# Kernel optimization log

Measured on AMD Instinct MI355X. Metric: run time of the kernel, lower is better.

## Reference

```python
import jax, jax.numpy as jnp
import numpy as np

EMB_DIM = 1024
N_HEADS = 16
HEAD_DIM = EMB_DIM // N_HEADS


def setup_inputs() -> dict:
    key = jax.random.key(0)
    ks = jax.random.split(key, 6)
    B, T, C = 2, 2048, EMB_DIM
    s = 1.0 / np.sqrt(C)
    return {
        "x": jax.random.normal(ks[0], (B, T, C), dtype=jnp.float32),
        "W_query": jax.random.normal(ks[1], (C, C), dtype=jnp.float32) * s,
        "W_key": jax.random.normal(ks[2], (C, C), dtype=jnp.float32) * s,
        "W_value": jax.random.normal(ks[3], (C, C), dtype=jnp.float32) * s,
        "W_out": jax.random.normal(ks[4], (C, C), dtype=jnp.float32) * s,
        "b_out": jax.random.normal(ks[5], (C,), dtype=jnp.float32) * 0.01,
    }


def reference(x, W_query, W_key, W_value, W_out, b_out):
    # x: [B, T, C]. Linear weights stored as [in, out] (transposed torch layout).
    B, T, C = x.shape
    H, D = N_HEADS, HEAD_DIM

    def split_heads(t):  # [B,T,C] -> [B,H,T,D]
        return t.reshape(B, T, H, D).transpose(0, 2, 1, 3)

    q = split_heads(x @ W_query)
    k = split_heads(x @ W_key)
    v = split_heads(x @ W_value)

    scale = 1.0 / jnp.sqrt(jnp.asarray(D, dtype=x.dtype))
    att = jnp.einsum("bhqd,bhkd->bhqk", q, k) * scale  # [B,H,T,T]
    causal = jnp.tril(jnp.ones((T, T), dtype=bool))
    att = jnp.where(causal[None, None], att, jnp.asarray(-jnp.inf, dtype=att.dtype))
    att = jax.nn.softmax(att, axis=-1)
    # dropout is identity in eval / drop_rate=0
    y = jnp.einsum("bhqk,bhkd->bhqd", att, v)  # [B,H,T,D]
    y = y.transpose(0, 2, 1, 3).reshape(B, T, C)
    return y @ W_out + b_out
```

## Files before the change

### kernel.cpp

```cpp
#include <hip/hip_runtime.h>
#include <hip/hip_bf16.h>
#include <math.h>

#define Bsz 2
#define Tsz 2048
#define Csz 1024
#define Hsz 16
#define Dsz 64

typedef __attribute__((ext_vector_type(8))) short frag8;
typedef __attribute__((ext_vector_type(4))) float f4;
typedef __attribute__((ext_vector_type(8))) unsigned short us8;
typedef __attribute__((ext_vector_type(4))) _Float16 frag4h;
typedef __attribute__((ext_vector_type(8))) _Float16 frag8h;

static __device__ __forceinline__ unsigned short f2bf(float f) {
  union { __hip_bfloat16 h; unsigned short u; } c;
  c.h = __float2bfloat16(f);
  return c.u;
}
static __device__ __forceinline__ unsigned short f2h(float f) {
  union { _Float16 h; unsigned short u; } c;
  c.h = (_Float16)f;
  return c.u;
}

#define GLDS16(g, l)                                                        \
  __builtin_amdgcn_global_load_lds(                                         \
      (const __attribute__((address_space(1))) void*)(g),                   \
      (__attribute__((address_space(3))) void*)(l), 16, 0, 0)

#define QSCALE 0.18033688f

__global__ __launch_bounds__(256) void cast_x(const float* __restrict__ x,
                                              unsigned short* __restrict__ xb) {
  const int i = (blockIdx.x * 256 + threadIdx.x) * 8;
  const float4 a = *(const float4*)(x + i);
  const float4 b = *(const float4*)(x + i + 4);
  us8 v;
  v[0] = f2bf(a.x); v[1] = f2bf(a.y); v[2] = f2bf(a.z); v[3] = f2bf(a.w);
  v[4] = f2bf(b.x); v[5] = f2bf(b.y); v[6] = f2bf(b.z); v[7] = f2bf(b.w);
  *(us8*)(xb + i) = v;
}

__global__ __launch_bounds__(256) void transpose_cast(
    const float* __restrict__ s0, const float* __restrict__ s1,
    const float* __restrict__ s2, const float* __restrict__ s3,
    unsigned short* __restrict__ d0, unsigned short* __restrict__ d1,
    unsigned short* __restrict__ d2, unsigned short* __restrict__ d3) {
  __shared__ float Ls[64][65];
  const int mat = blockIdx.x >> 8;
  const int tile = blockIdx.x & 255;
  const float* src = mat == 0 ? s0 : mat == 1 ? s1 : mat == 2 ? s2 : s3;
  unsigned short* dst = mat == 0 ? d0 : mat == 1 ? d1 : mat == 2 ? d2 : d3;
  const int tr0 = (tile >> 4) << 6, tc0 = (tile & 15) << 6;
  const int t = threadIdx.x;
  const int lr = t >> 4, lc = (t & 15) << 2;
#pragma unroll
  for (int j = 0; j < 4; ++j) {
    const float4 v = *(const float4*)(src + (size_t)(tr0 + lr + j * 16) * 1024 + tc0 + lc);
    Ls[lr + j * 16][lc + 0] = v.x;
    Ls[lr + j * 16][lc + 1] = v.y;
    Ls[lr + j * 16][lc + 2] = v.z;
    Ls[lr + j * 16][lc + 3] = v.w;
  }
  __syncthreads();
#pragma unroll
  for (int j = 0; j < 4; ++j) {
    ushort4 v;
    v.x = f2bf(Ls[lc + 0][lr + j * 16]);
    v.y = f2bf(Ls[lc + 1][lr + j * 16]);
    v.z = f2bf(Ls[lc + 2][lr + j * 16]);
    v.w = f2bf(Ls[lc + 3][lr + j * 16]);
    *(ushort4*)(dst + (size_t)(tc0 + lr + j * 16) * 1024 + tr0 + lc) = v;
  }
}

template <int MODE, int MT>
__global__ __launch_bounds__(256) void mm_bt(
    const unsigned short* __restrict__ A, const unsigned short* __restrict__ Bt,
    const float* __restrict__ bias, unsigned short* __restrict__ O0,
    unsigned short* __restrict__ O1, unsigned short* __restrict__ O2,
    float* __restrict__ Of) {
  __shared__ __align__(16) unsigned short As[MT * 32 * 64];
  __shared__ __align__(16) unsigned short Bs[128 * 64];
  const int K = 1024;
  const int tid = threadIdx.x;
  const int wave = tid >> 6, lane = tid & 63;
  const int quad = lane >> 4, l16 = lane & 15;
  const int wrow = (wave >> 1) * (MT * 16), wn = wave & 1;
  const int row0 = blockIdx.y * (MT * 32), col0 = blockIdx.x << 7;

  const int sr = lane >> 3, sg = lane & 7;
  const int g0 = sg ^ sr;
  const unsigned short* gA = A + (size_t)(row0 + wave * (MT * 8) + sr) * K + (g0 << 3);
  const unsigned short* gB = Bt + (size_t)(col0 + wave * 32 + sr) * K + (g0 << 3);

  f4 acc[MT][4];
#pragma unroll
  for (int i = 0; i < MT; ++i)
#pragma unroll
    for (int j = 0; j < 4; ++j) acc[i][j] = (f4){0.f, 0.f, 0.f, 0.f};

  for (int kk = 0; kk < K; kk += 64) {
    __syncthreads();
#pragma unroll
    for (int s = 0; s < MT; ++s)
      GLDS16(gA + kk + (size_t)(s * 8) * K, &As[(wave * (MT * 8) + s * 8) * 64]);
#pragma unroll
    for (int s = 0; s < 4; ++s)
      GLDS16(gB + kk + (size_t)(s * 8) * K, &Bs[(wave * 32 + s * 8) * 64]);
    __syncthreads();

#pragma unroll
    for (int ks = 0; ks < 2; ++ks) {
      frag8 af[MT], bf[4];
#pragma unroll
      for (int mt = 0; mt < MT; ++mt) {
        const int r = wrow + mt * 16 + l16;
        af[mt] = *(const frag8*)&As[r * 64 + (((ks * 4 + quad) ^ (l16 & 7)) << 3)];
      }
#pragma unroll
      for (int nt = 0; nt < 4; ++nt) {
        const int n = wn * 64 + nt * 16 + l16;
        bf[nt] = *(const frag8*)&Bs[n * 64 + (((ks * 4 + quad) ^ (l16 & 7)) << 3)];
      }
#pragma unroll
      for (int mt = 0; mt < MT; ++mt)
#pragma unroll
        for (int nt = 0; nt < 4; ++nt)
          acc[mt][nt] = __builtin_amdgcn_mfma_f32_16x16x32_bf16(af[mt], bf[nt], acc[mt][nt], 0, 0, 0);
    }
  }

  if (MODE == 0) {
    if (col0 < 2048) {
      const bool isK = (col0 >= 1024);
      unsigned short* dst = isK ? O1 : O0;
      const float sc = isK ? 1.0f : QSCALE;
#pragma unroll
      for (int mt = 0; mt < MT; ++mt)
#pragma unroll
        for (int nt = 0; nt < 4; ++nt) {
          const int m = row0 + wrow + mt * 16 + quad * 4;
          const int n = (col0 & 1023) + wn * 64 + nt * 16 + l16;
          const int b = m >> 11, h = n >> 6, d = n & 63;
#pragma unroll
          for (int r = 0; r < 4; ++r) {
            const int tk = (m + r) & (Tsz - 1);
            dst[(((size_t)b * Hsz + h) * Tsz + tk) * Dsz + d] = f2bf(acc[mt][nt][r] * sc);
          }
        }
    } else {
#pragma unroll
      for (int mt = 0; mt < MT; ++mt)
#pragma unroll
        for (int nt = 0; nt < 4; ++nt) {
          const int tok = row0 + wrow + mt * 16 + quad * 4;
          const int ch = (col0 - 2048) + wn * 64 + nt * 16 + l16;
          const int b = tok >> 11, tk = tok & (Tsz - 1);
          const int h = ch >> 6, d = ch & 63;
          const int t5 = tk & 31;
          const int pos = (tk & ~31) + ((t5 >> 4) << 2) + (((t5 >> 2) & 3) << 3) + (t5 & 3);
          ushort4 v;
          v.x = f2h(acc[mt][nt][0]); v.y = f2h(acc[mt][nt][1]);
          v.z = f2h(acc[mt][nt][2]); v.w = f2h(acc[mt][nt][3]);
          *(ushort4*)&O2[(((size_t)b * Hsz + h) * Dsz + d) * Tsz + pos] = v;
        }
    }
  } else {
#pragma unroll
    for (int mt = 0; mt < MT; ++mt)
#pragma unroll
      for (int nt = 0; nt < 4; ++nt) {
        const int m = row0 + wrow + mt * 16 + quad * 4;
        const int n = col0 + wn * 64 + nt * 16 + l16;
        const float bv = bias[n];
#pragma unroll
        for (int r = 0; r < 4; ++r)
          Of[(size_t)(m + r) * Csz + n] = acc[mt][nt][r] + bv;
      }
  }
}

__global__ __launch_bounds__(512, 4) void attn_mfma(
    const unsigned short* __restrict__ Qb,
    const unsigned short* __restrict__ Kb,
    const unsigned short* __restrict__ VTb,
    unsigned short* __restrict__ Y) {
  __shared__ __align__(16) unsigned char SMEM[65536];
#define KSP(spp, bb) ((unsigned short*)(SMEM + (spp) * 16384 + (bb) * 4096))
#define VSP(spp, bb) ((unsigned short*)(SMEM + (spp) * 16384 + 8192 + (bb) * 4096))

  const int tid = threadIdx.x;
  const int wave = tid >> 6, lane = tid & 63;
  const int quad = lane >> 4, l16 = lane & 15;
  const int t = wave & 1;
  const int sp = wave >> 1;
  const int ltid = tid & 127;

  const int bh = blockIdx.x & 31;
  const int pr = blockIdx.x >> 5;
  const int ja = pr, jb = 63 - pr;
  const int j = t ? jb : ja;
  const int qb0 = j << 5;

  const unsigned short* Qh = Qb + (size_t)bh * Tsz * Dsz;
  const unsigned short* Kh = Kb + (size_t)bh * Tsz * Dsz;
  const unsigned short* Vh = VTb + (size_t)bh * Dsz * Tsz;

  const int ke0 = ltid, ke1 = ltid + 128;
  const int kkey0 = ke0 >> 3, kc0 = ke0 & 7;
  const int kkey1 = ke1 >> 3, kc1 = ke1 & 7;
  const unsigned short* gK0 = Kh + (size_t)kkey0 * Dsz + ((kc0 ^ (kkey0 & 7)) << 3);
  const unsigned short* gK1 = Kh + (size_t)kkey1 * Dsz + ((kc1 ^ (kkey1 & 7)) << 3);
  const int vd0 = ltid >> 2, vc0 = ltid & 3;
  const int vd1 = vd0 + 32;
  const unsigned short* gV0 = Vh + (size_t)vd0 * Tsz + ((vc0 ^ ((vd0 + (vd0 >> 2)) & 3)) << 3);
  const unsigned short* gV1 = Vh + (size_t)vd1 * Tsz + ((vc0 ^ ((vd1 + (vd1 >> 2)) & 3)) << 3);
  const int wo = t * 512;

  frag8 qf[2][2];
#pragma unroll
  for (int m = 0; m < 2; ++m)
#pragma unroll
    for (int ks = 0; ks < 2; ++ks)
      qf[m][ks] = *(const frag8*)(Qh + (size_t)(qb0 + m * 16 + l16) * Dsz + ks * 32 + quad * 8);

  f4 o[2][4];
  float lsum[2] = {0.f, 0.f};
#pragma unroll
  for (int m = 0; m < 2; ++m)
#pragma unroll
    for (int nt = 0; nt < 4; ++nt) o[m][nt] = (f4){0.f, 0.f, 0.f, 0.f};
  const f4 zf = (f4){0.f, 0.f, 0.f, 0.f};
  const int fl = (l16 + (l16 >> 2)) & 3;

  const int nch = (jb >> 2) + 1;

  {
    const size_t kof0 = (size_t)(sp << 5) * Dsz, kof1 = (size_t)((sp + 4) << 5) * Dsz;
    const int vof0 = sp << 5, vof1 = (sp + 4) << 5;
    GLDS16(gK0 + kof0, KSP(sp, 0) + wo);
    GLDS16(gK1 + kof0, KSP(sp, 0) + wo + 1024);
    GLDS16(gV0 + vof0, VSP(sp, 0) + wo);
    GLDS16(gV1 + vof0, VSP(sp, 0) + wo + 1024);
    GLDS16(gK0 + kof1, KSP(sp, 1) + wo);
    GLDS16(gK1 + kof1, KSP(sp, 1) + wo + 1024);
    GLDS16(gV0 + vof1, VSP(sp, 1) + wo);
    GLDS16(gV1 + vof1, VSP(sp, 1) + wo + 1024);
  }
  __syncthreads();

  for (int i = 0; i < nch; ++i) {
    const int c = sp + 4 * i;
    const int bsel = i & 1;
    if (c <= j) {
      const unsigned short* Kl = KSP(sp, bsel);
      const unsigned short* Vl = VSP(sp, bsel);
      frag8 kf[2][2];
#pragma unroll
      for (int n = 0; n < 2; ++n)
#pragma unroll
        for (int ks = 0; ks < 2; ++ks)
          kf[n][ks] = *(const frag8*)&Kl[(n * 16 + l16) * 64 + (((ks * 4 + quad) ^ (l16 & 7)) << 3)];
      frag8h vf[4];
#pragma unroll
      for (int nt = 0; nt < 4; ++nt)
        vf[nt] = *(const frag8h*)&Vl[(nt * 16 + l16) * 32 + ((quad ^ fl) << 3)];

      f4 st[2][2];
#pragma unroll
      for (int n = 0; n < 2; ++n)
#pragma unroll
        for (int m = 0; m < 2; ++m) {
          f4 a = __builtin_amdgcn_mfma_f32_16x16x32_bf16(kf[n][0], qf[m][0], zf, 0, 0, 0);
          st[n][m] = __builtin_amdgcn_mfma_f32_16x16x32_bf16(kf[n][1], qf[m][1], a, 0, 0, 0);
        }
      const bool dm = (c == j);
      frag4h paf[2][2];
#pragma unroll
      for (int m = 0; m < 2; ++m) {
        const int qq = m * 16 + l16;
#pragma unroll
        for (int n = 0; n < 2; ++n) {
          const int key0 = n * 16 + quad * 4;
          float p[4];
#pragma unroll
          for (int r = 0; r < 4; ++r) {
            float sv = st[n][m][r];
            if (dm && (key0 + r > qq)) sv = -INFINITY;
            p[r] = __builtin_amdgcn_exp2f(sv);
          }
          lsum[m] += (p[0] + p[1]) + (p[2] + p[3]);
          frag4h ph;
          ph[0] = (_Float16)p[0]; ph[1] = (_Float16)p[1];
          ph[2] = (_Float16)p[2]; ph[3] = (_Float16)p[3];
          paf[m][n] = ph;
        }
      }
#pragma unroll
      for (int m = 0; m < 2; ++m)
#pragma unroll
        for (int nt = 0; nt < 4; ++nt) {
          const frag4h vlo = __builtin_shufflevector(vf[nt], vf[nt], 0, 1, 2, 3);
          const frag4h vhi = __builtin_shufflevector(vf[nt], vf[nt], 4, 5, 6, 7);
          f4 a = __builtin_amdgcn_mfma_f32_16x16x16f16(paf[m][0], vlo, o[m][nt], 0, 0, 0);
          o[m][nt] = __builtin_amdgcn_mfma_f32_16x16x16f16(paf[m][1], vhi, a, 0, 0, 0);
        }
    }
    __syncthreads();
    if (i + 2 < nch) {
      const int c2 = sp + 4 * (i + 2);
      const size_t kof = (size_t)(c2 << 5) * Dsz;
      const int vof = c2 << 5;
      GLDS16(gK0 + kof, KSP(sp, bsel) + wo);
      GLDS16(gK1 + kof, KSP(sp, bsel) + wo + 1024);
      GLDS16(gV0 + vof, VSP(sp, bsel) + wo);
      GLDS16(gV1 + vof, VSP(sp, bsel) + wo + 1024);
    }
  }

  float* comb = (float*)SMEM;
  const int slot = (sp - 1) * 2 + t;
  float* cp = comb + (size_t)(slot * 64 + lane) * 37;
  if (sp != 0) {
#pragma unroll
    for (int m = 0; m < 2; ++m)
#pragma unroll
      for (int nt = 0; nt < 4; ++nt)
        *(f4*)(cp + m * 16 + nt * 4) = o[m][nt];
    cp[32] = lsum[0]; cp[33] = lsum[1];
  }
  __syncthreads();
  if (sp == 0) {
#pragma unroll
    for (int s = 0; s < 3; ++s) {
      const float* rp = comb + (size_t)((s * 2 + t) * 64 + lane) * 37;
#pragma unroll
      for (int m = 0; m < 2; ++m)
#pragma unroll
        for (int nt = 0; nt < 4; ++nt)
          o[m][nt] += *(const f4*)(rp + m * 16 + nt * 4);
      lsum[0] += rp[32]; lsum[1] += rp[33];
    }

#pragma unroll
    for (int m = 0; m < 2; ++m) {
      lsum[m] += __shfl_xor(lsum[m], 16);
      lsum[m] += __shfl_xor(lsum[m], 32);
    }
    const int b = bh >> 4, h = bh & 15;
#pragma unroll
    for (int m = 0; m < 2; ++m)
#pragma unroll
      for (int r = 0; r < 4; ++r) {
        const float inv = 1.f / __shfl(lsum[m], quad * 4 + r);
        const int tk = qb0 + m * 16 + quad * 4 + r;
        unsigned short* yp = Y + ((size_t)b * Tsz + tk) * Csz + h * 64 + l16;
#pragma unroll
        for (int nt = 0; nt < 4; ++nt)
          yp[nt * 16] = f2bf(o[m][nt][r] * inv);
      }
  }
#undef KSP
#undef VSP
}

extern "C" void kernel_launch(void* const* d_in, const int* in_sizes, int n_in,
                              void* d_out, int out_size, void* d_ws, size_t ws_size,
                              hipStream_t stream) {
  const float* x  = (const float*)d_in[0];
  const float* Wq = (const float*)d_in[1];
  const float* Wk = (const float*)d_in[2];
  const float* Wv = (const float*)d_in[3];
  const float* Wo = (const float*)d_in[4];
  const float* bo = (const float*)d_in[5];

  const size_t NEL = (size_t)Bsz * Tsz * Csz;
  const size_t WSZ = (size_t)Csz * Csz;
  unsigned short* xb  = (unsigned short*)d_ws;
  unsigned short* WT  = xb + NEL;
  unsigned short* WoT = WT + 3 * WSZ;
  unsigned short* Qb  = WoT + WSZ;
  unsigned short* Kb  = Qb + NEL;
  unsigned short* VTb = Kb + NEL;
  unsigned short* Yb  = VTb + NEL;

  cast_x<<<NEL / 2048, 256, 0, stream>>>(x, xb);
  transpose_cast<<<1024, 256, 0, stream>>>(Wq, Wk, Wv, Wo,
                                           WT, WT + WSZ, WT + 2 * WSZ, WoT);

  mm_bt<0, 4><<<dim3(24, 32), 256, 0, stream>>>(xb, WT, nullptr, Qb, Kb, VTb, nullptr);

  attn_mfma<<<1024, 512, 0, stream>>>(Qb, Kb, VTb, Yb);

  mm_bt<2, 2><<<dim3(8, 64), 256, 0, stream>>>(Yb, WoT, bo, nullptr, nullptr, nullptr,
                                               (float*)d_out);
}
```

Before: 182.5 us.

## Load K/V fragments directly from global memory, dropping LDS double buffering

The attention kernel stops staging K and V chunks through LDS with async global_load_lds double buffering and per-iteration block barriers. Each wave now loads its MFMA K and V fragments straight from global memory (relying on cache), and the loop runs only over the chunks that wave needs. LDS shrinks to just the cross-wave combine buffer. The wave-to-(t,sp) mapping changes, and P is packed to f16 with cvt_pkrtz. This removes barrier stalls and LDS traffic but exposes global-load latency with no explicit prefetch, and it uses less coalesced fragment-shaped accesses.

Result: slower. 225.7 us (+23.7%).

```diff
diff --git a/kernel.cpp b/kernel.cpp
--- a/kernel.cpp
+++ b/kernel.cpp
@@ -13,6 +13,7 @@
 typedef __attribute__((ext_vector_type(8))) unsigned short us8;
 typedef __attribute__((ext_vector_type(4))) _Float16 frag4h;
 typedef __attribute__((ext_vector_type(8))) _Float16 frag8h;
+typedef __attribute__((ext_vector_type(2))) _Float16 h2;
 
 static __device__ __forceinline__ unsigned short f2bf(float f) {
   union { __hip_bfloat16 h; unsigned short u; } c;
@@ -188,16 +189,13 @@
     const unsigned short* __restrict__ Kb,
     const unsigned short* __restrict__ VTb,
     unsigned short* __restrict__ Y) {
-  __shared__ __align__(16) unsigned char SMEM[65536];
-#define KSP(spp, bb) ((unsigned short*)(SMEM + (spp) * 16384 + (bb) * 4096))
-#define VSP(spp, bb) ((unsigned short*)(SMEM + (spp) * 16384 + 8192 + (bb) * 4096))
+  __shared__ __align__(16) float comb[6 * 64 * 37];
 
   const int tid = threadIdx.x;
   const int wave = tid >> 6, lane = tid & 63;
   const int quad = lane >> 4, l16 = lane & 15;
-  const int t = wave & 1;
-  const int sp = wave >> 1;
-  const int ltid = tid & 127;
+  const int t = wave >> 2;
+  const int sp = wave & 3;
 
   const int bh = blockIdx.x & 31;
   const int pr = blockIdx.x >> 5;
@@ -209,17 +207,6 @@
   const unsigned short* Kh = Kb + (size_t)bh * Tsz * Dsz;
   const unsigned short* Vh = VTb + (size_t)bh * Dsz * Tsz;
 
-  const int ke0 = ltid, ke1 = ltid + 128;
-  const int kkey0 = ke0 >> 3, kc0 = ke0 & 7;
-  const int kkey1 = ke1 >> 3, kc1 = ke1 & 7;
-  const unsigned short* gK0 = Kh + (size_t)kkey0 * Dsz + ((kc0 ^ (kkey0 & 7)) << 3);
-  const unsigned short* gK1 = Kh + (size_t)kkey1 * Dsz + ((kc1 ^ (kkey1 & 7)) << 3);
-  const int vd0 = ltid >> 2, vc0 = ltid & 3;
-  const int vd1 = vd0 + 32;
-  const unsigned short* gV0 = Vh + (size_t)vd0 * Tsz + ((vc0 ^ ((vd0 + (vd0 >> 2)) & 3)) << 3);
-  const unsigned short* gV1 = Vh + (size_t)vd1 * Tsz + ((vc0 ^ ((vd1 + (vd1 >> 2)) & 3)) << 3);
-  const int wo = t * 512;
-
   frag8 qf[2][2];
 #pragma unroll
   for (int m = 0; m < 2; ++m)
@@ -234,94 +221,62 @@
 #pragma unroll
     for (int nt = 0; nt < 4; ++nt) o[m][nt] = (f4){0.f, 0.f, 0.f, 0.f};
   const f4 zf = (f4){0.f, 0.f, 0.f, 0.f};
-  const int fl = (l16 + (l16 >> 2)) & 3;
-
-  const int nch = (jb >> 2) + 1;
-
-  {
-    const size_t kof0 = (size_t)(sp << 5) * Dsz, kof1 = (size_t)((sp + 4) << 5) * Dsz;
-    const int vof0 = sp << 5, vof1 = (sp + 4) << 5;
-    GLDS16(gK0 + kof0, KSP(sp, 0) + wo);
-    GLDS16(gK1 + kof0, KSP(sp, 0) + wo + 1024);
-    GLDS16(gV0 + vof0, VSP(sp, 0) + wo);
-    GLDS16(gV1 + vof0, VSP(sp, 0) + wo + 1024);
-    GLDS16(gK0 + kof1, KSP(sp, 1) + wo);
-    GLDS16(gK1 + kof1, KSP(sp, 1) + wo + 1024);
-    GLDS16(gV0 + vof1, VSP(sp, 1) + wo);
-    GLDS16(gV1 + vof1, VSP(sp, 1) + wo + 1024);
-  }
-  __syncthreads();
-
-  for (int i = 0; i < nch; ++i) {
-    const int c = sp + 4 * i;
-    const int bsel = i & 1;
-    if (c <= j) {
-      const unsigned short* Kl = KSP(sp, bsel);
-      const unsigned short* Vl = VSP(sp, bsel);
-      frag8 kf[2][2];
-#pragma unroll
-      for (int n = 0; n < 2; ++n)
-#pragma unroll
-        for (int ks = 0; ks < 2; ++ks)
-          kf[n][ks] = *(const frag8*)&Kl[(n * 16 + l16) * 64 + (((ks * 4 + quad) ^ (l16 & 7)) << 3)];
-      frag8h vf[4];
-#pragma unroll
-      for (int nt = 0; nt < 4; ++nt)
-        vf[nt] = *(const frag8h*)&Vl[(nt * 16 + l16) * 32 + ((quad ^ fl) << 3)];
-
-      f4 st[2][2];
-#pragma unroll
-      for (int n = 0; n < 2; ++n)
-#pragma unroll
-        for (int m = 0; m < 2; ++m) {
-          f4 a = __builtin_amdgcn_mfma_f32_16x16x32_bf16(kf[n][0], qf[m][0], zf, 0, 0, 0);
-          st[n][m] = __builtin_amdgcn_mfma_f32_16x16x32_bf16(kf[n][1], qf[m][1], a, 0, 0, 0);
+
+  const unsigned short* kl = Kh + (size_t)l16 * Dsz + quad * 8;
+  const unsigned short* vl = Vh + (size_t)l16 * Tsz + quad * 8;
+
+  for (int c = sp; c <= j; c += 4) {
+    frag8 kf[2][2];
+#pragma unroll
+    for (int n = 0; n < 2; ++n)
+#pragma unroll
+      for (int ks = 0; ks < 2; ++ks)
+        kf[n][ks] = *(const frag8*)(kl + (size_t)(c * 32 + n * 16) * Dsz + ks * 32);
+    frag8h vf[4];
+#pragma unroll
+    for (int nt = 0; nt < 4; ++nt)
+      vf[nt] = *(const frag8h*)(vl + (size_t)(nt * 16) * Tsz + (c << 5));
+
+    f4 st[2][2];
+#pragma unroll
+    for (int n = 0; n < 2; ++n)
+#pragma unroll
+      for (int m = 0; m < 2; ++m) {
+        f4 a = __builtin_amdgcn_mfma_f32_16x16x32_bf16(kf[n][0], qf[m][0], zf, 0, 0, 0);
+        st[n][m] = __builtin_amdgcn_mfma_f32_16x16x32_bf16(kf[n][1], qf[m][1], a, 0, 0, 0);
+      }
+    const bool dm = (c == j);
+    frag4h paf[2][2];
+#pragma unroll
+    for (int m = 0; m < 2; ++m) {
+      const int qq = m * 16 + l16;
+#pragma unroll
+      for (int n = 0; n < 2; ++n) {
+        const int key0 = n * 16 + quad * 4;
+        float p[4];
+#pragma unroll
+        for (int r = 0; r < 4; ++r) {
+          float sv = st[n][m][r];
+          if (dm && (key0 + r > qq)) sv = -INFINITY;
+          p[r] = __builtin_amdgcn_exp2f(sv);
         }
-      const bool dm = (c == j);
-      frag4h paf[2][2];
-#pragma unroll
-      for (int m = 0; m < 2; ++m) {
-        const int qq = m * 16 + l16;
-#pragma unroll
-        for (int n = 0; n < 2; ++n) {
-          const int key0 = n * 16 + quad * 4;
-          float p[4];
-#pragma unroll
-          for (int r = 0; r < 4; ++r) {
-            float sv = st[n][m][r];
-            if (dm && (key0 + r > qq)) sv = -INFINITY;
-            p[r] = __builtin_amdgcn_exp2f(sv);
-          }
-          lsum[m] += (p[0] + p[1]) + (p[2] + p[3]);
-          frag4h ph;
-          ph[0] = (_Float16)p[0]; ph[1] = (_Float16)p[1];
-          ph[2] = (_Float16)p[2]; ph[3] = (_Float16)p[3];
-          paf[m][n] = ph;
-        }
-      }
-#pragma unroll
-      for (int m = 0; m < 2; ++m)
-#pragma unroll
-        for (int nt = 0; nt < 4; ++nt) {
-          const frag4h vlo = __builtin_shufflevector(vf[nt], vf[nt], 0, 1, 2, 3);
-          const frag4h vhi = __builtin_shufflevector(vf[nt], vf[nt], 4, 5, 6, 7);
-          f4 a = __builtin_amdgcn_mfma_f32_16x16x16f16(paf[m][0], vlo, o[m][nt], 0, 0, 0);
-          o[m][nt] = __builtin_amdgcn_mfma_f32_16x16x16f16(paf[m][1], vhi, a, 0, 0, 0);
-        }
-    }
-    __syncthreads();
-    if (i + 2 < nch) {
-      const int c2 = sp + 4 * (i + 2);
-      const size_t kof = (size_t)(c2 << 5) * Dsz;
-      const int vof = c2 << 5;
-      GLDS16(gK0 + kof, KSP(sp, bsel) + wo);
-      GLDS16(gK1 + kof, KSP(sp, bsel) + wo + 1024);
-      GLDS16(gV0 + vof, VSP(sp, bsel) + wo);
-      GLDS16(gV1 + vof, VSP(sp, bsel) + wo + 1024);
-    }
-  }
-
-  float* comb = (float*)SMEM;
+        lsum[m] += (p[0] + p[1]) + (p[2] + p[3]);
+        const h2 lo = __builtin_bit_cast(h2, __builtin_amdgcn_cvt_pkrtz(p[0], p[1]));
+        const h2 hi = __builtin_bit_cast(h2, __builtin_amdgcn_cvt_pkrtz(p[2], p[3]));
+        paf[m][n] = __builtin_shufflevector(lo, hi, 0, 1, 2, 3);
+      }
+    }
+#pragma unroll
+    for (int m = 0; m < 2; ++m)
+#pragma unroll
+      for (int nt = 0; nt < 4; ++nt) {
+        const frag4h vlo = __builtin_shufflevector(vf[nt], vf[nt], 0, 1, 2, 3);
+        const frag4h vhi = __builtin_shufflevector(vf[nt], vf[nt], 4, 5, 6, 7);
+        f4 a = __builtin_amdgcn_mfma_f32_16x16x16f16(paf[m][0], vlo, o[m][nt], 0, 0, 0);
+        o[m][nt] = __builtin_amdgcn_mfma_f32_16x16x16f16(paf[m][1], vhi, a, 0, 0, 0);
+      }
+  }
+
   const int slot = (sp - 1) * 2 + t;
   float* cp = comb + (size_t)(slot * 64 + lane) * 37;
   if (sp != 0) {
@@ -363,8 +318,6 @@
           yp[nt * 16] = f2bf(o[m][nt][r] * inv);
       }
   }
-#undef KSP
-#undef VSP
 }
 
 extern "C" void kernel_launch(void* const* d_in, const int* in_sizes, int n_in,
```

## Split both causal query tiles across wave pair to balance work

Applied to the files above, without the earlier changes.

Previously each wave pair had one wave handle the short query tile (ja) and the other the long tile (jb), so one wave sat idle for most chunks. Now each wave takes 16 query rows from both tiles: it always computes the jb tile and also the ja tile while the chunk is within its range. This evens out work between waves and shortens the critical path per block. In exchange each wave holds more registers for two accumulator sets, and the reduction and store code are reorganised to match.

New measurement: 180.7 us. Within noise of the previous version (-1.0%).

```diff
diff --git a/kernel.cpp b/kernel.cpp
--- a/kernel.cpp
+++ b/kernel.cpp
@@ -202,8 +202,7 @@
   const int bh = blockIdx.x & 31;
   const int pr = blockIdx.x >> 5;
   const int ja = pr, jb = 63 - pr;
-  const int j = t ? jb : ja;
-  const int qb0 = j << 5;
+  const int qa0 = ja << 5, qb0 = jb << 5;
 
   const unsigned short* Qh = Qb + (size_t)bh * Tsz * Dsz;
   const unsigned short* Kh = Kb + (size_t)bh * Tsz * Dsz;
@@ -220,21 +219,23 @@
   const unsigned short* gV1 = Vh + (size_t)vd1 * Tsz + ((vc0 ^ ((vd1 + (vd1 >> 2)) & 3)) << 3);
   const int wo = t * 512;
 
-  frag8 qf[2][2];
-#pragma unroll
-  for (int m = 0; m < 2; ++m)
-#pragma unroll
-    for (int ks = 0; ks < 2; ++ks)
-      qf[m][ks] = *(const frag8*)(Qh + (size_t)(qb0 + m * 16 + l16) * Dsz + ks * 32 + quad * 8);
-
-  f4 o[2][4];
-  float lsum[2] = {0.f, 0.f};
-#pragma unroll
-  for (int m = 0; m < 2; ++m)
-#pragma unroll
-    for (int nt = 0; nt < 4; ++nt) o[m][nt] = (f4){0.f, 0.f, 0.f, 0.f};
+  frag8 qfa[2], qfb[2];
+#pragma unroll
+  for (int ks = 0; ks < 2; ++ks) {
+    qfa[ks] = *(const frag8*)(Qh + (size_t)(qa0 + t * 16 + l16) * Dsz + ks * 32 + quad * 8);
+    qfb[ks] = *(const frag8*)(Qh + (size_t)(qb0 + t * 16 + l16) * Dsz + ks * 32 + quad * 8);
+  }
+
+  f4 oa[4], ob[4];
+  float lsa = 0.f, lsb = 0.f;
+#pragma unroll
+  for (int nt = 0; nt < 4; ++nt) {
+    oa[nt] = (f4){0.f, 0.f, 0.f, 0.f};
+    ob[nt] = (f4){0.f, 0.f, 0.f, 0.f};
+  }
   const f4 zf = (f4){0.f, 0.f, 0.f, 0.f};
   const int fl = (l16 + (l16 >> 2)) & 3;
+  const int qq = t * 16 + l16;
 
   const int nch = (jb >> 2) + 1;
 
@@ -255,7 +256,7 @@
   for (int i = 0; i < nch; ++i) {
     const int c = sp + 4 * i;
     const int bsel = i & 1;
-    if (c <= j) {
+    if (c <= jb) {
       const unsigned short* Kl = KSP(sp, bsel);
       const unsigned short* Vl = VSP(sp, bsel);
       frag8 kf[2][2];
@@ -269,45 +270,72 @@
       for (int nt = 0; nt < 4; ++nt)
         vf[nt] = *(const frag8h*)&Vl[(nt * 16 + l16) * 32 + ((quad ^ fl) << 3)];
 
-      f4 st[2][2];
-#pragma unroll
-      for (int n = 0; n < 2; ++n)
-#pragma unroll
-        for (int m = 0; m < 2; ++m) {
-          f4 a = __builtin_amdgcn_mfma_f32_16x16x32_bf16(kf[n][0], qf[m][0], zf, 0, 0, 0);
-          st[n][m] = __builtin_amdgcn_mfma_f32_16x16x32_bf16(kf[n][1], qf[m][1], a, 0, 0, 0);
-        }
-      const bool dm = (c == j);
-      frag4h paf[2][2];
-#pragma unroll
-      for (int m = 0; m < 2; ++m) {
-        const int qq = m * 16 + l16;
+      {
+        f4 st[2];
+#pragma unroll
+        for (int n = 0; n < 2; ++n) {
+          f4 a = __builtin_amdgcn_mfma_f32_16x16x32_bf16(kf[n][0], qfb[0], zf, 0, 0, 0);
+          st[n] = __builtin_amdgcn_mfma_f32_16x16x32_bf16(kf[n][1], qfb[1], a, 0, 0, 0);
+        }
+        const bool dm = (c == jb);
+        frag4h paf[2];
 #pragma unroll
         for (int n = 0; n < 2; ++n) {
           const int key0 = n * 16 + quad * 4;
           float p[4];
 #pragma unroll
           for (int r = 0; r < 4; ++r) {
-            float sv = st[n][m][r];
+            float sv = st[n][r];
             if (dm && (key0 + r > qq)) sv = -INFINITY;
             p[r] = __builtin_amdgcn_exp2f(sv);
           }
-          lsum[m] += (p[0] + p[1]) + (p[2] + p[3]);
+          lsb += (p[0] + p[1]) + (p[2] + p[3]);
           frag4h ph;
           ph[0] = (_Float16)p[0]; ph[1] = (_Float16)p[1];
           ph[2] = (_Float16)p[2]; ph[3] = (_Float16)p[3];
-          paf[m][n] = ph;
-        }
-      }
-#pragma unroll
-      for (int m = 0; m < 2; ++m)
+          paf[n] = ph;
+        }
 #pragma unroll
         for (int nt = 0; nt < 4; ++nt) {
           const frag4h vlo = __builtin_shufflevector(vf[nt], vf[nt], 0, 1, 2, 3);
           const frag4h vhi = __builtin_shufflevector(vf[nt], vf[nt], 4, 5, 6, 7);
-          f4 a = __builtin_amdgcn_mfma_f32_16x16x16f16(paf[m][0], vlo, o[m][nt], 0, 0, 0);
-          o[m][nt] = __builtin_amdgcn_mfma_f32_16x16x16f16(paf[m][1], vhi, a, 0, 0, 0);
-        }
+          f4 a = __builtin_amdgcn_mfma_f32_16x16x16f16(paf[0], vlo, ob[nt], 0, 0, 0);
+          ob[nt] = __builtin_amdgcn_mfma_f32_16x16x16f16(paf[1], vhi, a, 0, 0, 0);
+        }
+      }
+      if (c <= ja) {
+        f4 st[2];
+#pragma unroll
+        for (int n = 0; n < 2; ++n) {
+          f4 a = __builtin_amdgcn_mfma_f32_16x16x32_bf16(kf[n][0], qfa[0], zf, 0, 0, 0);
+          st[n] = __builtin_amdgcn_mfma_f32_16x16x32_bf16(kf[n][1], qfa[1], a, 0, 0, 0);
+        }
+        const bool dm = (c == ja);
+        frag4h paf[2];
+#pragma unroll
+        for (int n = 0; n < 2; ++n) {
+          const int key0 = n * 16 + quad * 4;
+          float p[4];
+#pragma unroll
+          for (int r = 0; r < 4; ++r) {
+            float sv = st[n][r];
+            if (dm && (key0 + r > qq)) sv = -INFINITY;
+            p[r] = __builtin_amdgcn_exp2f(sv);
+          }
+          lsa += (p[0] + p[1]) + (p[2] + p[3]);
+          frag4h ph;
+          ph[0] = (_Float16)p[0]; ph[1] = (_Float16)p[1];
+          ph[2] = (_Float16)p[2]; ph[3] = (_Float16)p[3];
+          paf[n] = ph;
+        }
+#pragma unroll
+        for (int nt = 0; nt < 4; ++nt) {
+          const frag4h vlo = __builtin_shufflevector(vf[nt], vf[nt], 0, 1, 2, 3);
+          const frag4h vhi = __builtin_shufflevector(vf[nt], vf[nt], 4, 5, 6, 7);
+          f4 a = __builtin_amdgcn_mfma_f32_16x16x16f16(paf[0], vlo, oa[nt], 0, 0, 0);
+          oa[nt] = __builtin_amdgcn_mfma_f32_16x16x16f16(paf[1], vhi, a, 0, 0, 0);
+        }
+      }
     }
     __syncthreads();
     if (i + 2 < nch) {
@@ -326,11 +354,11 @@
   float* cp = comb + (size_t)(slot * 64 + lane) * 37;
   if (sp != 0) {
 #pragma unroll
-    for (int m = 0; m < 2; ++m)
-#pragma unroll
-      for (int nt = 0; nt < 4; ++nt)
-        *(f4*)(cp + m * 16 + nt * 4) = o[m][nt];
-    cp[32] = lsum[0]; cp[33] = lsum[1];
+    for (int nt = 0; nt < 4; ++nt) {
+      *(f4*)(cp + nt * 4) = oa[nt];
+      *(f4*)(cp + 16 + nt * 4) = ob[nt];
+    }
+    cp[32] = lsa; cp[33] = lsb;
   }
   __syncthreads();
   if (sp == 0) {
@@ -338,30 +366,34 @@
     for (int s = 0; s < 3; ++s) {
       const float* rp = comb + (size_t)((s * 2 + t) * 64 + lane) * 37;
 #pragma unroll
-      for (int m = 0; m < 2; ++m)
-#pragma unroll
-        for (int nt = 0; nt < 4; ++nt)
-          o[m][nt] += *(const f4*)(rp + m * 16 + nt * 4);
-      lsum[0] += rp[32]; lsum[1] += rp[33];
-    }
-
-#pragma unroll
-    for (int m = 0; m < 2; ++m) {
-      lsum[m] += __shfl_xor(lsum[m], 16);
-      lsum[m] += __shfl_xor(lsum[m], 32);
-    }
+      for (int nt = 0; nt < 4; ++nt) {
+        oa[nt] += *(const f4*)(rp + nt * 4);
+        ob[nt] += *(const f4*)(rp + 16 + nt * 4);
+      }
+      lsa += rp[32]; lsb += rp[33];
+    }
+
+    lsa += __shfl_xor(lsa, 16); lsa += __shfl_xor(lsa, 32);
+    lsb += __shfl_xor(lsb, 16); lsb += __shfl_xor(lsb, 32);
     const int b = bh >> 4, h = bh & 15;
 #pragma unroll
-    for (int m = 0; m < 2; ++m)
-#pragma unroll
-      for (int r = 0; r < 4; ++r) {
-        const float inv = 1.f / __shfl(lsum[m], quad * 4 + r);
-        const int tk = qb0 + m * 16 + quad * 4 + r;
-        unsigned short* yp = Y + ((size_t)b * Tsz + tk) * Csz + h * 64 + l16;
-#pragma unroll
-        for (int nt = 0; nt < 4; ++nt)
-          yp[nt * 16] = f2bf(o[m][nt][r] * inv);
-      }
+    for (int r = 0; r < 4; ++r) {
+      const float inv = 1.f / __shfl(lsa, quad * 4 + r);
+      const int tk = qa0 + t * 16 + quad * 4 + r;
+      unsigned short* yp = Y + ((size_t)b * Tsz + tk) * Csz + h * 64 + l16;
+#pragma unroll
+      for (int nt = 0; nt < 4; ++nt)
+        yp[nt * 16] = f2bf(oa[nt][r] * inv);
+    }
+#pragma unroll
+    for (int r = 0; r < 4; ++r) {
+      const float inv = 1.f / __shfl(lsb, quad * 4 + r);
+      const int tk = qb0 + t * 16 + quad * 4 + r;
+      unsigned short* yp = Y + ((size_t)b * Tsz + tk) * Csz + h * 64 + l16;
+#pragma unroll
+      for (int nt = 0; nt < 4; ++nt)
+        yp[nt * 16] = f2bf(ob[nt][r] * inv);
+    }
   }
 #undef KSP
 #undef VSP
```
